# Performance work log

Measured on AMD Instinct MI355X. Metric: run time of the kernel, lower is better.

Reference implementation:

```python
import jax, jax.numpy as jnp
import numpy as np

MB, NK, DM, DT = 4096, 8, 1024, 128
EPS = 1e-3  # LayerNormalization eps, added to sigma OUTSIDE sqrt


def setup_inputs() -> dict:
    key = jax.random.key(0)
    ks = jax.random.split(key, 7)
    xav = lambda fan_in, fan_out: (2.0 / (fan_in + fan_out)) ** 0.5
    return {
        "q": jax.random.normal(ks[0], (MB, NK, DM), jnp.float32),
        "k": jax.random.normal(ks[1], (MB, NK, DM), jnp.float32),
        "v": jax.random.normal(ks[2], (MB, NK, DM), jnp.float32),
        "w_qs": jax.random.normal(ks[3], (NK, DM, DT), jnp.float32) * xav(DM, DT),
        "w_ks": jax.random.normal(ks[4], (NK, DM, DT), jnp.float32) * xav(DM, DT),
        "w_vs": jax.random.normal(ks[5], (NK, DM, DT), jnp.float32) * xav(DM, DT),
        # torch Linear: weight [out, in] = [NK*DM, NK*DT]
        "proj_w": jax.random.normal(ks[6], (NK * DM, NK * DT), jnp.float32) * xav(NK * DT, NK * DM),
        "proj_b": jnp.zeros((NK * DM,), jnp.float32),
        "gamma": jnp.ones((DM,), jnp.float32),
        "beta": jnp.zeros((DM,), jnp.float32),
    }


def reference(q, k, v, w_qs, w_ks, w_vs, proj_w, proj_b, gamma, beta):
    mb, nk, dm = q.shape
    dt = w_qs.shape[-1]
    residual = v

    # torch: q.view(n_kernel, mb, d_model) on contiguous [mb, nk, dm] == raw reshape
    q_s = jnp.einsum('nbd,ndt->nbt', q.reshape(nk, mb, dm), w_qs)  # [nk, mb, dt]
    k_s = jnp.einsum('nbd,ndt->nbt', k.reshape(nk, mb, dm), w_ks)
    v_s = jnp.einsum('nbd,ndt->nbt', v.reshape(nk, mb, dm), w_vs)

    # ScaledDotProductAttention on [nk*mb, 1, dt] -> scores [.,1,1]; softmax over
    # a singleton dim is identically 1, so output == v_s (faithful to source).
    temper = np.float32(np.sqrt(dm))
    scores = jnp.sum(q_s * k_s, axis=-1) / temper            # [nk, mb]
    attn = jax.nn.softmax(scores[:, :, None, None], axis=-1)  # [nk, mb, 1, 1] == 1.0
    out = attn[..., 0] * v_s                                  # [nk, mb, dt]
    attns = attn.reshape(nk * mb, 1, 1)

    # torch .view(mb, nk*dt) on the [nk, mb, dt]-contiguous buffer (raw reshape)
    outputs = out.reshape(mb, nk * dt)
    outputs = outputs @ proj_w.T + proj_b                     # [mb, nk*dm]
    z = outputs.reshape(mb, nk, dm) + residual

    # custom LayerNormalization: unbiased std, eps outside sqrt
    mu = jnp.mean(z, axis=-1, keepdims=True)
    sigma = jnp.std(z, axis=-1, keepdims=True, ddof=1)
    output = (z - mu) / (sigma + EPS) * gamma + beta
    return (output, attns)
```

## Files before the change

### kernel.cpp

```cpp
#include <hip/hip_runtime.h>
#include <cstdint>
#include <cstddef>

#define MB_   4096
#define NK_   8
#define DM_   1024
#define DT_   128

typedef __bf16 bf16;
typedef __bf16 bf16x8 __attribute__((ext_vector_type(8)));
typedef __bf16 bf16x4 __attribute__((ext_vector_type(4)));
typedef float  f32x4  __attribute__((ext_vector_type(4)));

__device__ __forceinline__ void gload_lds16(const void* g, void* l) {
  __builtin_amdgcn_global_load_lds(
      (__attribute__((address_space(1))) void*)g,
      (__attribute__((address_space(3))) void*)l,
      16, 0, 0);
}

__device__ __forceinline__ int hsw(int r) { return (r ^ (r >> 2)) & 3; }

__global__ void prep_kernel(const float* __restrict__ pw, bf16* __restrict__ pwb,
                            const float* __restrict__ wvs, bf16* __restrict__ wvt) {
  int b = blockIdx.x;
  if (b < 8192) {
    size_t i = ((size_t)b * 256 + threadIdx.x) * 4;
    float4 f = *(const float4*)&pw[i];
    bf16x4 o = { (bf16)f.x, (bf16)f.y, (bf16)f.z, (bf16)f.w };
    *(bf16x4*)&pwb[i] = o;
  } else {
    int o = (b - 8192) * 256 + threadIdx.x;
    int d = o & 1023;
    int t = (o >> 10) & 127;
    int n = o >> 17;
    wvt[o] = (bf16)wvs[(size_t)n * 131072 + (size_t)d * 128 + t];
  }
}

__global__ __launch_bounds__(256, 2) void gemm1_kernel(
    const float* __restrict__ vflat, const bf16* __restrict__ WvT,
    bf16* __restrict__ A2)
{
  __shared__ __align__(16) bf16 As[64 * 32];
  __shared__ __align__(16) bf16 Bs[128 * 32];
  const int tid  = threadIdx.x;
  const int wave = tid >> 6, lane = tid & 63;
  const int wm = wave >> 1, wn = wave & 1;
  const int n  = blockIdx.y;
  const int b0 = blockIdx.x * 64;

  const int r  = tid >> 2;
  const int hr = hsw(r);
  const int cs = (tid & 3) ^ hr;

  const float* ag = vflat + ((size_t)(n * MB_ + b0 + r)) * 1024 + (tid & 3) * 8;
  bf16* awr = As + r * 32 + cs * 8;
  const bf16* bg = WvT + (size_t)n * 131072 + (size_t)r * 1024 + cs * 8;
  char* bsb = (char*)Bs + wave * 1024;

  f32x4 acc[2][4] = {};
  const int krow = lane & 15;
  const int cch  = lane >> 4;
  const int swoff = ((cch ^ hsw(krow)) << 4);

  for (int kt = 0; kt < 32; ++kt) {
    const bf16* bptr = bg + kt * 32;
    gload_lds16(bptr,             bsb);
    gload_lds16(bptr + 64 * 1024, bsb + 4096);
    const float* aptr = ag + kt * 32;
    float4 f0 = *(const float4*)(aptr + 0);
    float4 f1 = *(const float4*)(aptr + 4);
    bf16x8 h0 = { (bf16)f0.x, (bf16)f0.y, (bf16)f0.z, (bf16)f0.w,
                  (bf16)f1.x, (bf16)f1.y, (bf16)f1.z, (bf16)f1.w };
    *(bf16x8*)awr = h0;
    __syncthreads();

    bf16x8 af[2], bfr[4];
    #pragma unroll
    for (int i = 0; i < 2; ++i)
      af[i] = *(const bf16x8*)((const char*)As + (wm * 32 + i * 16 + krow) * 64 + swoff);
    #pragma unroll
    for (int j = 0; j < 4; ++j)
      bfr[j] = *(const bf16x8*)((const char*)Bs + (wn * 64 + j * 16 + krow) * 64 + swoff);
    #pragma unroll
    for (int i = 0; i < 2; ++i)
      #pragma unroll
      for (int j = 0; j < 4; ++j)
        acc[i][j] = __builtin_amdgcn_mfma_f32_16x16x32_bf16(af[i], bfr[j], acc[i][j], 0, 0, 0);
    __syncthreads();
  }

  #pragma unroll
  for (int i = 0; i < 2; ++i) {
    #pragma unroll
    for (int j = 0; j < 4; ++j) {
      int t = wn * 64 + j * 16 + (lane & 15);
      #pragma unroll
      for (int rr = 0; rr < 4; ++rr) {
        int b = b0 + wm * 32 + i * 16 + (lane >> 4) * 4 + rr;
        size_t off = ((size_t)(n * 512 + (b >> 3))) * 1024 + (size_t)(b & 7) * 128 + t;
        A2[off] = (bf16)acc[i][j][rr];
      }
    }
  }
}

template<bool ZB>
__global__ __launch_bounds__(512, 2) void gemm2c_kernel(
    const bf16* __restrict__ A2, const bf16* __restrict__ PW,
    const float* __restrict__ pb, void* __restrict__ xoutp)
{
  __shared__ __align__(16) bf16 As[4][8192];
  __shared__ __align__(16) bf16 Bs[4][8192];

  const int tid  = threadIdx.x;
  const int w    = tid >> 6;
  const int lane = tid & 63;
  const int wm   = w >> 2;
  const int wn   = w & 3;

  const int bid   = blockIdx.x;
  const int x     = bid & 7;
  const int local = bid >> 3;
  const int mt    = local & 15;
  const int nt    = x * 4 + (local >> 4);
  const int m0    = mt * 256;
  const int n0    = nt * 256;

  const int rS = tid >> 2;
  const int cS = (tid & 3) ^ hsw(rS);
  const char* aG0 = (const char*)A2 + (size_t)(m0 + rS) * 2048 + cS * 16;
  const char* aG1 = aG0 + (size_t)128 * 2048;
  const char* bG0 = (const char*)PW + (size_t)(n0 + rS) * 2048 + cS * 16;
  const char* bG1 = bG0 + (size_t)128 * 2048;

  #define STAGE(t) { char* dA = (char*)As[(t) & 3] + tid * 16;               \
                     char* dB = (char*)Bs[(t) & 3] + tid * 16;               \
                     gload_lds16(aG0 + (size_t)(t) * 64, dA);                \
                     gload_lds16(aG1 + (size_t)(t) * 64, dA + 8192);         \
                     gload_lds16(bG0 + (size_t)(t) * 64, dB);                \
                     gload_lds16(bG1 + (size_t)(t) * 64, dB + 8192); }

  STAGE(0); STAGE(1); STAGE(2);
  asm volatile("s_waitcnt vmcnt(8)" ::: "memory");
  __builtin_amdgcn_s_barrier();
  __builtin_amdgcn_sched_barrier(0);

  f32x4 acc[8][4] = {};
  const int fr = lane & 15;
  const int g  = lane >> 4;
  const int swoff = ((g ^ hsw(fr)) << 4);
  const int aRd = (wm * 128 + fr) * 64 + swoff;
  const int bRd = (wn * 64  + fr) * 64 + swoff;

  #pragma unroll 1
  for (int s = 0; s < 32; ++s) {
    if (s < 29) STAGE(s + 3);

    const char* pA = (const char*)As[s & 3] + aRd;
    const char* pB = (const char*)Bs[s & 3] + bRd;
    bf16x8 a[8], b[4];
    #pragma unroll
    for (int m = 0; m < 8; ++m) a[m] = *(const bf16x8*)(pA + m * 1024);
    #pragma unroll
    for (int n = 0; n < 4; ++n) b[n] = *(const bf16x8*)(pB + n * 1024);
    #pragma unroll
    for (int m = 0; m < 8; ++m)
      #pragma unroll
      for (int n = 0; n < 4; ++n)
        acc[m][n] = __builtin_amdgcn_mfma_f32_16x16x32_bf16(a[m], b[n], acc[m][n], 0, 0, 0);

    asm volatile("s_waitcnt lgkmcnt(0)" ::: "memory");
    if (s < 29)       { asm volatile("s_waitcnt vmcnt(8)" ::: "memory"); }
    else if (s == 29) { asm volatile("s_waitcnt vmcnt(4)" ::: "memory"); }
    else if (s == 30) { asm volatile("s_waitcnt vmcnt(0)" ::: "memory"); }
    __builtin_amdgcn_s_barrier();
    __builtin_amdgcn_sched_barrier(0);
  }
  #undef STAGE

  #pragma unroll
  for (int m = 0; m < 8; ++m) {
    #pragma unroll
    for (int n = 0; n < 4; ++n) {
      int nn = n0 + wn * 64 + n * 16 + fr;
      float pbn = pb[nn];
      #pragma unroll
      for (int r = 0; r < 4; ++r) {
        int mm = m0 + wm * 128 + m * 16 + g * 4 + r;
        size_t off = (size_t)mm * 8192 + nn;
        float val = acc[m][n][r] + pbn;
        if (ZB) ((bf16*)xoutp)[off] = (bf16)val;
        else    ((float*)xoutp)[off] = val;
      }
    }
  }
}

template<bool ZB>
__global__ __launch_bounds__(256) void ln_kernel(
    const void* zin, const float* __restrict__ vres,
    const float* __restrict__ gamma, const float* __restrict__ beta,
    float* outp)
{
  __shared__ float red[16];
  const int row = blockIdx.x;
  const int tid = threadIdx.x;
  if (row < 128) outp[(size_t)33554432 + row * 256 + tid] = 1.0f;
  const size_t base = (size_t)row * 1024 + tid * 4;

  float4 rv = *(const float4*)&vres[base];
  float4 x;
  if (ZB) {
    bf16x4 zb4 = *(const bf16x4*)((const bf16*)zin + base);
    x.x = (float)zb4[0] + rv.x; x.y = (float)zb4[1] + rv.y;
    x.z = (float)zb4[2] + rv.z; x.w = (float)zb4[3] + rv.w;
  } else {
    float4 zf = *(const float4*)((const float*)zin + base);
    x.x = zf.x + rv.x; x.y = zf.y + rv.y; x.z = zf.z + rv.z; x.w = zf.w + rv.w;
  }

  float s  = x.x + x.y + x.z + x.w;
  float ss = x.x * x.x + x.y * x.y + x.z * x.z + x.w * x.w;
  #pragma unroll
  for (int m = 32; m >= 1; m >>= 1) {
    s  += __shfl_xor(s,  m, 64);
    ss += __shfl_xor(ss, m, 64);
  }
  const int wave = tid >> 6, lane = tid & 63;
  if (lane == 0) { red[wave] = s; red[wave + 8] = ss; }
  __syncthreads();
  float S  = red[0] + red[1] + red[2] + red[3];
  float SS = red[8] + red[9] + red[10] + red[11];
  float mu  = S * (1.0f / 1024.0f);
  float var = (SS - 1024.0f * mu * mu) * (1.0f / 1023.0f);
  var = var < 0.0f ? 0.0f : var;
  float rs = 1.0f / (sqrtf(var) + 1e-3f);
  float4 gmv = *(const float4*)&gamma[tid * 4];
  float4 be  = *(const float4*)&beta[tid * 4];
  float4 y;
  y.x = (x.x - mu) * rs * gmv.x + be.x;
  y.y = (x.y - mu) * rs * gmv.y + be.y;
  y.z = (x.z - mu) * rs * gmv.z + be.z;
  y.w = (x.w - mu) * rs * gmv.w + be.w;
  *(float4*)&outp[base] = y;
}

extern "C" void kernel_launch(void* const* d_in, const int* in_sizes, int n_in,
                              void* d_out, int out_size, void* d_ws, size_t ws_size,
                              hipStream_t stream) {
  const float* v     = (const float*)d_in[2];
  const float* wvs   = (const float*)d_in[5];
  const float* pw    = (const float*)d_in[6];
  const float* pb    = (const float*)d_in[7];
  const float* gamma = (const float*)d_in[8];
  const float* beta  = (const float*)d_in[9];
  float* out = (float*)d_out;

  const size_t OFF_WVT = 16777216;
  const size_t OFF_A2  = OFF_WVT + 2097152;
  const size_t OFF_X   = OFF_A2 + 8388608;
  const size_t NEED_ZB = OFF_X + 67108864;

  bf16* PWb = (bf16*)d_ws;
  bf16* WvT = (bf16*)((char*)d_ws + OFF_WVT);
  bf16* A2  = (bf16*)((char*)d_ws + OFF_A2);
  const bool zb = (ws_size >= NEED_ZB);
  void* xbuf = zb ? (void*)((char*)d_ws + OFF_X) : (void*)out;

  hipLaunchKernelGGL(prep_kernel, dim3(12288), dim3(256), 0, stream, pw, PWb, wvs, WvT);
  hipLaunchKernelGGL(gemm1_kernel, dim3(64, 8), dim3(256), 0, stream, v, WvT, A2);
  if (zb) {
    hipLaunchKernelGGL((gemm2c_kernel<true>),  dim3(512), dim3(512), 0, stream, A2, PWb, pb, xbuf);
    hipLaunchKernelGGL((ln_kernel<true>),      dim3(32768), dim3(256), 0, stream, xbuf, v, gamma, beta, out);
  } else {
    hipLaunchKernelGGL((gemm2c_kernel<false>), dim3(512), dim3(512), 0, stream, A2, PWb, pb, xbuf);
    hipLaunchKernelGGL((ln_kernel<false>),     dim3(32768), dim3(256), 0, stream, xbuf, v, gamma, beta, out);
  }
}
```

Before: 209.1 us.

## Use 1024-thread blocks with 64x64 per-wave tiles in output projection GEMM

Doubles the GEMM2 block to 16 waves so each wave computes a 64x64 sub-tile of the 256x256 output tile, halving per-thread global-to-LDS loads and accumulator registers. The aim is more waves in flight to hide memory latency. In exchange, each MFMA needs more LDS fragment reads and barriers span more waves. The trailing barrier on the last iteration is dropped.

```diff
diff --git a/kernel.cpp b/kernel.cpp
--- a/kernel.cpp
+++ b/kernel.cpp
@@ -107,7 +107,7 @@
 }
 
 template<bool ZB>
-__global__ __launch_bounds__(512, 2) void gemm2c_kernel(
+__global__ __launch_bounds__(1024, 4) void gemm2v_kernel(
     const bf16* __restrict__ A2, const bf16* __restrict__ PW,
     const float* __restrict__ pb, void* __restrict__ xoutp)
 {
@@ -130,67 +130,66 @@
 
   const int rS = tid >> 2;
   const int cS = (tid & 3) ^ hsw(rS);
-  const char* aG0 = (const char*)A2 + (size_t)(m0 + rS) * 2048 + cS * 16;
-  const char* aG1 = aG0 + (size_t)128 * 2048;
-  const char* bG0 = (const char*)PW + (size_t)(n0 + rS) * 2048 + cS * 16;
-  const char* bG1 = bG0 + (size_t)128 * 2048;
-
-  #define STAGE(t) { char* dA = (char*)As[(t) & 3] + tid * 16;               \
-                     char* dB = (char*)Bs[(t) & 3] + tid * 16;               \
-                     gload_lds16(aG0 + (size_t)(t) * 64, dA);                \
-                     gload_lds16(aG1 + (size_t)(t) * 64, dA + 8192);         \
-                     gload_lds16(bG0 + (size_t)(t) * 64, dB);                \
-                     gload_lds16(bG1 + (size_t)(t) * 64, dB + 8192); }
+  const char* aG = (const char*)A2 + (size_t)(m0 + rS) * 2048 + cS * 16;
+  const char* bG = (const char*)PW + (size_t)(n0 + rS) * 2048 + cS * 16;
+
+  #define STAGE(t) { gload_lds16(aG + (size_t)(t) * 64, (char*)As[(t) & 3] + tid * 16); \
+                     gload_lds16(bG + (size_t)(t) * 64, (char*)Bs[(t) & 3] + tid * 16); }
 
   STAGE(0); STAGE(1); STAGE(2);
-  asm volatile("s_waitcnt vmcnt(8)" ::: "memory");
+  asm volatile("s_waitcnt vmcnt(4)" ::: "memory");
   __builtin_amdgcn_s_barrier();
   __builtin_amdgcn_sched_barrier(0);
 
-  f32x4 acc[8][4] = {};
+  f32x4 acc[4][4] = {};
   const int fr = lane & 15;
   const int g  = lane >> 4;
-  const int swoff = ((g ^ hsw(fr)) << 4);
-  const int aRd = (wm * 128 + fr) * 64 + swoff;
-  const int bRd = (wn * 64  + fr) * 64 + swoff;
 
   #pragma unroll 1
-  for (int s = 0; s < 32; ++s) {
-    if (s < 29) STAGE(s + 3);
-
-    const char* pA = (const char*)As[s & 3] + aRd;
-    const char* pB = (const char*)Bs[s & 3] + bRd;
-    bf16x8 a[8], b[4];
-    #pragma unroll
-    for (int m = 0; m < 8; ++m) a[m] = *(const bf16x8*)(pA + m * 1024);
-    #pragma unroll
-    for (int n = 0; n < 4; ++n) b[n] = *(const bf16x8*)(pB + n * 1024);
-    #pragma unroll
-    for (int m = 0; m < 8; ++m)
-      #pragma unroll
-      for (int n = 0; n < 4; ++n)
-        acc[m][n] = __builtin_amdgcn_mfma_f32_16x16x32_bf16(a[m], b[n], acc[m][n], 0, 0, 0);
-
-    asm volatile("s_waitcnt lgkmcnt(0)" ::: "memory");
-    if (s < 29)       { asm volatile("s_waitcnt vmcnt(8)" ::: "memory"); }
-    else if (s == 29) { asm volatile("s_waitcnt vmcnt(4)" ::: "memory"); }
-    else if (s == 30) { asm volatile("s_waitcnt vmcnt(0)" ::: "memory"); }
-    __builtin_amdgcn_s_barrier();
-    __builtin_amdgcn_sched_barrier(0);
-  }
+  for (int t = 0; t < 32; ++t) {
+    if (t < 29) STAGE(t + 3);
+
+    const char* pA = (const char*)As[t & 3];
+    const char* pB = (const char*)Bs[t & 3];
+    bf16x8 a[4], b[4];
+    #pragma unroll
+    for (int i = 0; i < 4; ++i) {
+      int r = wm * 64 + i * 16 + fr;
+      a[i] = *(const bf16x8*)(pA + r * 64 + ((g ^ hsw(r)) << 4));
+    }
+    #pragma unroll
+    for (int j = 0; j < 4; ++j) {
+      int r = wn * 64 + j * 16 + fr;
+      b[j] = *(const bf16x8*)(pB + r * 64 + ((g ^ hsw(r)) << 4));
+    }
+    #pragma unroll
+    for (int i = 0; i < 4; ++i)
+      #pragma unroll
+      for (int j = 0; j < 4; ++j)
+        acc[i][j] = __builtin_amdgcn_mfma_f32_16x16x32_bf16(a[i], b[j], acc[i][j], 0, 0, 0);
+
+    if (t < 31) {
+      asm volatile("s_waitcnt lgkmcnt(0)" ::: "memory");
+      if (t < 29)       { asm volatile("s_waitcnt vmcnt(4)" ::: "memory"); }
+      else if (t == 29) { asm volatile("s_waitcnt vmcnt(2)" ::: "memory"); }
+      else              { asm volatile("s_waitcnt vmcnt(0)" ::: "memory"); }
+      __builtin_amdgcn_s_barrier();
+      __builtin_amdgcn_sched_barrier(0);
+    }
+    }
   #undef STAGE
 
   #pragma unroll
-  for (int m = 0; m < 8; ++m) {
-    #pragma unroll
-    for (int n = 0; n < 4; ++n) {
-      int nn = n0 + wn * 64 + n * 16 + fr;
+  for (int i = 0; i < 4; ++i) {
+    #pragma unroll
+    for (int j = 0; j < 4; ++j) {
+      int nn = n0 + wn * 64 + j * 16 + fr;
       float pbn = pb[nn];
       #pragma unroll
       for (int r = 0; r < 4; ++r) {
-        int mm = m0 + wm * 128 + m * 16 + g * 4 + r;
+        int mm = m0 + wm * 64 + i * 16 + g * 4 + r;
         size_t off = (size_t)mm * 8192 + nn;
-        float val = acc[m][n][r] + pbn;
+        float val = acc[i][j][r] + pbn;
         if (ZB) ((bf16*)xoutp)[off] = (bf16)val;
         else    ((float*)xoutp)[off] = val;
       }
@@ -272,10 +271,10 @@
   hipLaunchKernelGGL(prep_kernel, dim3(12288), dim3(256), 0, stream, pw, PWb, wvs, WvT);
   hipLaunchKernelGGL(gemm1_kernel, dim3(64, 8), dim3(256), 0, stream, v, WvT, A2);
   if (zb) {
-    hipLaunchKernelGGL((gemm2c_kernel<true>),  dim3(512), dim3(512), 0, stream, A2, PWb, pb, xbuf);
+    hipLaunchKernelGGL((gemm2v_kernel<true>),  dim3(512), dim3(1024), 0, stream, A2, PWb, pb, xbuf);
     hipLaunchKernelGGL((ln_kernel<true>),      dim3(32768), dim3(256), 0, stream, xbuf, v, gamma, beta, out);
   } else {
-    hipLaunchKernelGGL((gemm2c_kernel<false>), dim3(512), dim3(512), 0, stream, A2, PWb, pb, xbuf);
+    hipLaunchKernelGGL((gemm2v_kernel<false>), dim3(512), dim3(1024), 0, stream, A2, PWb, pb, xbuf);
     hipLaunchKernelGGL((ln_kernel<false>),     dim3(32768), dim3(256), 0, stream, xbuf, v, gamma, beta, out);
   }
 }
```

After: 197.9 us. 5.4% less time.

## Restructure gemm2 main loop into split-phase pipeline with setprio and staggered loads

Applied to the files above, without the earlier changes.

The projection GEMM loop now uses a 2-stage-ahead prefetch instead of 3. Each k-step is split into two half-phases, and A/B loads are interleaved with MFMA blocks. Barriers and s_setprio raise wave priority around the MFMA clusters, in the style of ping-pong scheduling. The attns=1.0 fill moves out of the layernorm kernel into extra blocks of the prep kernel. The new schedule adds barriers per iteration and shortens prefetch depth, which could expose more memory latency.

```diff
diff --git a/kernel.cpp b/kernel.cpp
--- a/kernel.cpp
+++ b/kernel.cpp
@@ -22,19 +22,23 @@
 __device__ __forceinline__ int hsw(int r) { return (r ^ (r >> 2)) & 3; }
 
 __global__ void prep_kernel(const float* __restrict__ pw, bf16* __restrict__ pwb,
-                            const float* __restrict__ wvs, bf16* __restrict__ wvt) {
+                            const float* __restrict__ wvs, bf16* __restrict__ wvt,
+                            float* __restrict__ out) {
   int b = blockIdx.x;
+  int tid = threadIdx.x;
   if (b < 8192) {
-    size_t i = ((size_t)b * 256 + threadIdx.x) * 4;
+    size_t i = ((size_t)b * 256 + tid) * 4;
     float4 f = *(const float4*)&pw[i];
     bf16x4 o = { (bf16)f.x, (bf16)f.y, (bf16)f.z, (bf16)f.w };
     *(bf16x4*)&pwb[i] = o;
-  } else {
-    int o = (b - 8192) * 256 + threadIdx.x;
+  } else if (b < 12288) {
+    int o = (b - 8192) * 256 + tid;
     int d = o & 1023;
     int t = (o >> 10) & 127;
     int n = o >> 17;
     wvt[o] = (bf16)wvs[(size_t)n * 131072 + (size_t)d * 128 + t];
+  } else {
+    out[(size_t)33554432 + (size_t)(b - 12288) * 256 + tid] = 1.0f;
   }
 }
 
@@ -107,7 +111,7 @@
 }
 
 template<bool ZB>
-__global__ __launch_bounds__(512, 2) void gemm2c_kernel(
+__global__ __launch_bounds__(512, 2) void gemm2p_kernel(
     const bf16* __restrict__ A2, const bf16* __restrict__ PW,
     const float* __restrict__ pb, void* __restrict__ xoutp)
 {
@@ -135,17 +139,17 @@
   const char* bG0 = (const char*)PW + (size_t)(n0 + rS) * 2048 + cS * 16;
   const char* bG1 = bG0 + (size_t)128 * 2048;
 
-  #define STAGE(t) { char* dA = (char*)As[(t) & 3] + tid * 16;               \
-                     char* dB = (char*)Bs[(t) & 3] + tid * 16;               \
-                     gload_lds16(aG0 + (size_t)(t) * 64, dA);                \
-                     gload_lds16(aG1 + (size_t)(t) * 64, dA + 8192);         \
-                     gload_lds16(bG0 + (size_t)(t) * 64, dB);                \
-                     gload_lds16(bG1 + (size_t)(t) * 64, dB + 8192); }
-
-  STAGE(0); STAGE(1); STAGE(2);
-  asm volatile("s_waitcnt vmcnt(8)" ::: "memory");
+  #define STAGE_A(t) { char* d = (char*)As[(t) & 3] + tid * 16;            \
+                       gload_lds16(aG0 + (t) * 64, d);                      \
+                       gload_lds16(aG1 + (t) * 64, d + 8192); }
+  #define STAGE_B(t) { char* d = (char*)Bs[(t) & 3] + tid * 16;            \
+                       gload_lds16(bG0 + (t) * 64, d);                      \
+                       gload_lds16(bG1 + (t) * 64, d + 8192); }
+
+  STAGE_A(0); STAGE_B(0); STAGE_A(1); STAGE_B(1);
+  asm volatile("s_waitcnt vmcnt(4)" ::: "memory");
+  __builtin_amdgcn_sched_barrier(0);
   __builtin_amdgcn_s_barrier();
-  __builtin_amdgcn_sched_barrier(0);
 
   f32x4 acc[8][4] = {};
   const int fr = lane & 15;
@@ -154,31 +158,46 @@
   const int aRd = (wm * 128 + fr) * 64 + swoff;
   const int bRd = (wn * 64  + fr) * 64 + swoff;
 
-  #pragma unroll 1
-  for (int s = 0; s < 32; ++s) {
-    if (s < 29) STAGE(s + 3);
-
-    const char* pA = (const char*)As[s & 3] + aRd;
-    const char* pB = (const char*)Bs[s & 3] + bRd;
-    bf16x8 a[8], b[4];
-    #pragma unroll
-    for (int m = 0; m < 8; ++m) a[m] = *(const bf16x8*)(pA + m * 1024);
+  #pragma unroll 4
+  for (int t = 0; t < 32; ++t) {
+    const char* pA = (const char*)As[t & 3] + aRd;
+    const char* pB = (const char*)Bs[t & 3] + bRd;
+
+    bf16x8 a[4], b[4];
+    #pragma unroll
+    for (int m = 0; m < 4; ++m) a[m] = *(const bf16x8*)(pA + m * 1024);
     #pragma unroll
     for (int n = 0; n < 4; ++n) b[n] = *(const bf16x8*)(pB + n * 1024);
-    #pragma unroll
-    for (int m = 0; m < 8; ++m)
+    if (t < 30) STAGE_A(t + 2);
+    __builtin_amdgcn_s_barrier();
+    __builtin_amdgcn_s_setprio(1);
+    #pragma unroll
+    for (int m = 0; m < 4; ++m)
       #pragma unroll
       for (int n = 0; n < 4; ++n)
         acc[m][n] = __builtin_amdgcn_mfma_f32_16x16x32_bf16(a[m], b[n], acc[m][n], 0, 0, 0);
-
-    asm volatile("s_waitcnt lgkmcnt(0)" ::: "memory");
-    if (s < 29)       { asm volatile("s_waitcnt vmcnt(8)" ::: "memory"); }
-    else if (s == 29) { asm volatile("s_waitcnt vmcnt(4)" ::: "memory"); }
-    else if (s == 30) { asm volatile("s_waitcnt vmcnt(0)" ::: "memory"); }
-    __builtin_amdgcn_s_barrier();
+    __builtin_amdgcn_s_setprio(0);
+    __builtin_amdgcn_s_barrier();
+
+    bf16x8 a2[4];
+    #pragma unroll
+    for (int m = 0; m < 4; ++m) a2[m] = *(const bf16x8*)(pA + (4 + m) * 1024);
+    if (t < 30) STAGE_B(t + 2);
+    __builtin_amdgcn_s_barrier();
+    __builtin_amdgcn_s_setprio(1);
+    #pragma unroll
+    for (int m = 0; m < 4; ++m)
+      #pragma unroll
+      for (int n = 0; n < 4; ++n)
+        acc[4 + m][n] = __builtin_amdgcn_mfma_f32_16x16x32_bf16(a2[m], b[n], acc[4 + m][n], 0, 0, 0);
+    __builtin_amdgcn_s_setprio(0);
+    if (t < 30)       { asm volatile("s_waitcnt vmcnt(4)" ::: "memory"); }
+    else if (t == 30) { asm volatile("s_waitcnt vmcnt(0)" ::: "memory"); }
     __builtin_amdgcn_sched_barrier(0);
-  }
-  #undef STAGE
+    __builtin_amdgcn_s_barrier();
+  }
+  #undef STAGE_A
+  #undef STAGE_B
 
   #pragma unroll
   for (int m = 0; m < 8; ++m) {
@@ -207,7 +226,6 @@
   __shared__ float red[16];
   const int row = blockIdx.x;
   const int tid = threadIdx.x;
-  if (row < 128) outp[(size_t)33554432 + row * 256 + tid] = 1.0f;
   const size_t base = (size_t)row * 1024 + tid * 4;
 
   float4 rv = *(const float4*)&vres[base];
@@ -269,13 +287,13 @@
   const bool zb = (ws_size >= NEED_ZB);
   void* xbuf = zb ? (void*)((char*)d_ws + OFF_X) : (void*)out;
 
-  hipLaunchKernelGGL(prep_kernel, dim3(12288), dim3(256), 0, stream, pw, PWb, wvs, WvT);
+  hipLaunchKernelGGL(prep_kernel, dim3(12416), dim3(256), 0, stream, pw, PWb, wvs, WvT, out);
   hipLaunchKernelGGL(gemm1_kernel, dim3(64, 8), dim3(256), 0, stream, v, WvT, A2);
   if (zb) {
-    hipLaunchKernelGGL((gemm2c_kernel<true>),  dim3(512), dim3(512), 0, stream, A2, PWb, pb, xbuf);
+    hipLaunchKernelGGL((gemm2p_kernel<true>),  dim3(512), dim3(512), 0, stream, A2, PWb, pb, xbuf);
     hipLaunchKernelGGL((ln_kernel<true>),      dim3(32768), dim3(256), 0, stream, xbuf, v, gamma, beta, out);
   } else {
-    hipLaunchKernelGGL((gemm2c_kernel<false>), dim3(512), dim3(512), 0, stream, A2, PWb, pb, xbuf);
+    hipLaunchKernelGGL((gemm2p_kernel<false>), dim3(512), dim3(512), 0, stream, A2, PWb, pb, xbuf);
     hipLaunchKernelGGL((ln_kernel<false>),     dim3(32768), dim3(256), 0, stream, xbuf, v, gamma, beta, out);
   }
 }
```

After: 196.7 us. 5.9% less time.
